# Kernel tuning notes

Measured on AMD Instinct MI355X. Metric: run time of the kernel, lower is better.

The kernel has to match this reference:

```python
import jax, jax.numpy as jnp
import numpy as np

NUM_EMBEDDINGS = 1024
EMBEDDING_DIM = 128
COMMITMENT_COST = 0.25


def setup_inputs() -> dict:
    key = jax.random.key(0)
    k_in, k_cb = jax.random.split(key)
    inputs = jax.random.normal(k_in, (65536, EMBEDDING_DIM), dtype=jnp.float32)
    # torch init: uniform(-1/K, 1/K)
    codebook = jax.random.uniform(
        k_cb, (NUM_EMBEDDINGS, EMBEDDING_DIM), dtype=jnp.float32,
        minval=-1.0 / NUM_EMBEDDINGS, maxval=1.0 / NUM_EMBEDDINGS)
    return {"inputs": inputs, "codebook": codebook}


def reference(inputs, codebook):
    # inputs: [N, D], codebook: [K, D]
    # squared euclidean distances [N, K]
    distances = (jnp.sum(inputs ** 2, axis=1, keepdims=True)
                 + jnp.sum(codebook ** 2, axis=1)
                 - 2.0 * jnp.matmul(inputs, codebook.T))
    encoding_indices = jnp.argmin(distances, axis=1)  # [N]
    encodings = jax.nn.one_hot(encoding_indices, NUM_EMBEDDINGS, dtype=jnp.float32)  # [N, K]
    # onehot @ codebook == gather
    quantized = jnp.take(codebook, encoding_indices, axis=0)  # [N, D]

    e_latent_loss = jnp.mean((jax.lax.stop_gradient(quantized) - inputs) ** 2)
    q_latent_loss = jnp.mean((quantized - jax.lax.stop_gradient(inputs)) ** 2)
    loss = q_latent_loss + COMMITMENT_COST * e_latent_loss

    # straight-through estimator
    quantized_st = inputs + jax.lax.stop_gradient(quantized - inputs)

    avg_probs = jnp.mean(encodings, axis=0)  # [K]
    perplexity = jnp.exp(-jnp.sum(avg_probs * jnp.log(avg_probs + 1e-10)))
    return (loss, quantized_st, perplexity, encodings)
```

## Files before the change

kernel.cpp:

```cpp
#include <hip/hip_runtime.h>

#define NROWS 65536
#define DIM   128
#define KC    1024
#define QST_OFF  1
#define PPL_OFF  8388609
#define ENC_OFF  8388610

typedef float f32x2 __attribute__((ext_vector_type(2)));
typedef float floatx4 __attribute__((ext_vector_type(4)));
typedef _Float16 half8_t __attribute__((ext_vector_type(8)));
typedef _Float16 half4_t __attribute__((ext_vector_type(4)));

#define BSTR 144
#define TILEH (64 * BSTR)
#define CHUNKH (2 * TILEH)

__device__ __forceinline__ float fadd_rn_(float a, float b) {
#pragma clang fp contract(off)
  return a + b;
}
__device__ __forceinline__ float fsub_rn_(float a, float b) {
#pragma clang fp contract(off)
  return a - b;
}
__device__ __forceinline__ float fmul_rn_(float a, float b) {
#pragma clang fp contract(off)
  return a * b;
}

__device__ __forceinline__ float rowsq128(const float4* src) {
  float r[8];
  {
    float4 v0 = src[0], v1 = src[1];
    r[0] = fmul_rn_(v0.x, v0.x); r[1] = fmul_rn_(v0.y, v0.y);
    r[2] = fmul_rn_(v0.z, v0.z); r[3] = fmul_rn_(v0.w, v0.w);
    r[4] = fmul_rn_(v1.x, v1.x); r[5] = fmul_rn_(v1.y, v1.y);
    r[6] = fmul_rn_(v1.z, v1.z); r[7] = fmul_rn_(v1.w, v1.w);
  }
  for (int i = 1; i < 16; ++i) {
    float4 v0 = src[2 * i], v1 = src[2 * i + 1];
    r[0] = fadd_rn_(r[0], fmul_rn_(v0.x, v0.x));
    r[1] = fadd_rn_(r[1], fmul_rn_(v0.y, v0.y));
    r[2] = fadd_rn_(r[2], fmul_rn_(v0.z, v0.z));
    r[3] = fadd_rn_(r[3], fmul_rn_(v0.w, v0.w));
    r[4] = fadd_rn_(r[4], fmul_rn_(v1.x, v1.x));
    r[5] = fadd_rn_(r[5], fmul_rn_(v1.y, v1.y));
    r[6] = fadd_rn_(r[6], fmul_rn_(v1.z, v1.z));
    r[7] = fadd_rn_(r[7], fmul_rn_(v1.w, v1.w));
  }
  return fadd_rn_(fadd_rn_(fadd_rn_(r[0], r[1]), fadd_rn_(r[2], r[3])),
                  fadd_rn_(fadd_rn_(r[4], r[5]), fadd_rn_(r[6], r[7])));
}

__global__ __launch_bounds__(256) void k_prep(const float* __restrict__ cb,
                                              float* __restrict__ cbT,
                                              float* __restrict__ cc,
                                              _Float16* __restrict__ Bp) {
  __shared__ float tile[64 * 129];
  int t = threadIdx.x;
  int c0 = blockIdx.x * 64;
#pragma unroll
  for (int it = 0; it < 32; ++it) {
    int f = it * 256 + t;
    int c = f >> 7, d = f & 127;
    tile[c * 129 + d] = cb[(size_t)(c0 + c) * DIM + d];
  }
  __syncthreads();
#pragma unroll
  for (int it = 0; it < 32; ++it) {
    int f = it * 256 + t;
    int d = f >> 6, c = f & 63;
    cbT[(size_t)d * KC + c0 + c] = tile[c * 129 + d];
  }
  if (t < 64) {
    const float* s = &tile[t * 129];
    float r[8];
#pragma unroll
    for (int j = 0; j < 8; ++j) r[j] = fmul_rn_(s[j], s[j]);
    for (int i = 1; i < 16; ++i) {
#pragma unroll
      for (int j = 0; j < 8; ++j)
        r[j] = fadd_rn_(r[j], fmul_rn_(s[i * 8 + j], s[i * 8 + j]));
    }
    cc[c0 + t] = fadd_rn_(fadd_rn_(fadd_rn_(r[0], r[1]), fadd_rn_(r[2], r[3])),
                          fadd_rn_(fadd_rn_(r[4], r[5]), fadd_rn_(r[6], r[7])));
  }
  size_t base = (size_t)blockIdx.x * CHUNKH;
#pragma unroll
  for (int it = 0; it < 32; ++it) {
    int f = it * 256 + t;
    int c = f >> 7, k = f & 127;
    float c5 = tile[c * 129 + k] * 512.0f;
    _Float16 h = (_Float16)c5;
    _Float16 l = (_Float16)(c5 - (float)h);
    Bp[base + c * BSTR + k] = h;
    Bp[base + TILEH + c * BSTR + k] = l;
  }
}

__global__ __launch_bounds__(256, 4) void k_main(const float* __restrict__ inp,
                                                 const float* __restrict__ cb,
                                                 const float* __restrict__ cbT,
                                                 const _Float16* __restrict__ Bp,
                                                 const float* __restrict__ cc,
                                                 float* __restrict__ out_qst,
                                                 float* __restrict__ out_enc,
                                                 int* __restrict__ cnt,
                                                 float* __restrict__ lsum) {
  __shared__ _Float16 SB[CHUNKH];
  __shared__ float xxs[64];
  __shared__ int bk[64];
  __shared__ int fl_rows[64];
  __shared__ int fl_cnt;
  __shared__ float xs[128];
  __shared__ float redd[4];
  __shared__ int redi[4];
  __shared__ float redf[4];

  int t = threadIdx.x;
  int lane = t & 63, w = t >> 6;
  int q = lane >> 4, col = lane & 15;
  int row0 = blockIdx.x * 64;
  if (t == 0) fl_cnt = 0;

  {
    int r = t & 63, seg = t >> 6;
    const float* src = inp + (size_t)(row0 + r) * DIM + seg * 32;
#pragma unroll
    for (int i = 0; i < 8; ++i) {
      float4 v = *(const float4*)(src + i * 4);
      _Float16 h0 = (_Float16)v.x, h1 = (_Float16)v.y, h2 = (_Float16)v.z, h3 = (_Float16)v.w;
      half4_t hv = {h0, h1, h2, h3};
      half4_t lv = {(_Float16)(v.x - (float)h0), (_Float16)(v.y - (float)h1),
                    (_Float16)(v.z - (float)h2), (_Float16)(v.w - (float)h3)};
      int k = seg * 32 + i * 4;
      *(half4_t*)&SB[r * BSTR + k] = hv;
      *(half4_t*)&SB[TILEH + r * BSTR + k] = lv;
    }
  }
  if (t < 64) xxs[t] = rowsq128((const float4*)(inp + (size_t)(row0 + t) * DIM));
  __syncthreads();

  int arow = w * 16 + col;
  half8_t ah[4], al[4];
#pragma unroll
  for (int ks = 0; ks < 4; ++ks) {
    ah[ks] = *(const half8_t*)&SB[arow * BSTR + ks * 32 + q * 8];
    al[ks] = *(const half8_t*)&SB[TILEH + arow * BSTR + ks * 32 + q * 8];
  }
  float xr[4];
#pragma unroll
  for (int r = 0; r < 4; ++r) xr[r] = xxs[w * 16 + q * 4 + r];

  float b1[4], b2[4];
  int i1[4];
#pragma unroll
  for (int r = 0; r < 4; ++r) { b1[r] = 3.4e38f; b2[r] = 3.4e38f; i1[r] = 0; }

  const float4* bp4 = (const float4*)Bp;

  for (int c = 0; c < 16; ++c) {
    __syncthreads();
    {
      float4 br[9];
#pragma unroll
      for (int r = 0; r < 9; ++r) br[r] = bp4[c * 2304 + r * 256 + t];
#pragma unroll
      for (int r = 0; r < 9; ++r) *(float4*)&SB[(size_t)(r * 256 + t) * 8] = br[r];
    }
    __syncthreads();

    float cck[4];
#pragma unroll
    for (int ct = 0; ct < 4; ++ct) cck[ct] = cc[c * 64 + ct * 16 + col];

    floatx4 acc[4];
#pragma unroll
    for (int ct = 0; ct < 4; ++ct) acc[ct] = (floatx4){0.f, 0.f, 0.f, 0.f};

#pragma unroll
    for (int ks = 0; ks < 4; ++ks) {
#pragma unroll
      for (int ct = 0; ct < 4; ++ct) {
        int brow = ct * 16 + col;
        half8_t bh = *(const half8_t*)&SB[brow * BSTR + ks * 32 + q * 8];
        half8_t bl = *(const half8_t*)&SB[TILEH + brow * BSTR + ks * 32 + q * 8];
        acc[ct] = __builtin_amdgcn_mfma_f32_16x16x32_f16(ah[ks], bh, acc[ct], 0, 0, 0);
        acc[ct] = __builtin_amdgcn_mfma_f32_16x16x32_f16(ah[ks], bl, acc[ct], 0, 0, 0);
        acc[ct] = __builtin_amdgcn_mfma_f32_16x16x32_f16(al[ks], bh, acc[ct], 0, 0, 0);
      }
    }

#pragma unroll
    for (int ct = 0; ct < 4; ++ct) {
#pragma unroll
      for (int r = 0; r < 4; ++r) {
        float m2 = fmul_rn_(acc[ct][r], 0.00390625f);
        float dist = fsub_rn_(fadd_rn_(xr[r], cck[ct]), m2);
        int kidx = c * 64 + ct * 16 + col;
        bool lt = dist < b1[r];
        b2[r] = lt ? b1[r] : fminf(b2[r], dist);
        i1[r] = lt ? kidx : i1[r];
        b1[r] = lt ? dist : b1[r];
      }
    }
  }

#pragma unroll
  for (int r = 0; r < 4; ++r) {
    float v1 = b1[r], v2 = b2[r];
    int ii = i1[r];
    for (int off = 1; off < 16; off <<= 1) {
      float ov1 = __shfl_xor(v1, off);
      float ov2 = __shfl_xor(v2, off);
      int oi = __shfl_xor(ii, off);
      float nb1 = fminf(v1, ov1);
      float nb2 = fminf(fmaxf(v1, ov1), fminf(v2, ov2));
      ii = (ov1 < v1) ? oi : ((ov1 > v1) ? ii : min(ii, oi));
      v1 = nb1; v2 = nb2;
    }
    b1[r] = v1; b2[r] = v2; i1[r] = ii;
  }

  if (col == 0) {
#pragma unroll
    for (int r = 0; r < 4; ++r) {
      int lrow = w * 16 + q * 4 + r;
      bk[lrow] = i1[r];
      float u = (b1[r] >= 256.f) ? 9.4e-5f : 4.7e-5f;
      if (b2[r] - b1[r] < u) {
        int p = atomicAdd(&fl_cnt, 1);
        fl_rows[p] = lrow;
      }
    }
  }
  __syncthreads();

  int nf = fl_cnt;
  for (int f = 0; f < nf; ++f) {
    int row = fl_rows[f];
    if (t < 128) xs[t] = inp[(size_t)(row0 + row) * DIM + t];
    __syncthreads();
    float xxr = xxs[row];
    int c0 = t * 4;
    float a0 = 0.f, a1 = 0.f, a2 = 0.f, a3 = 0.f;
    for (int d = 0; d < 128; ++d) {
      float xd = xs[d];
      float4 cv = *(const float4*)&cbT[(size_t)d * KC + c0];
      a0 = __builtin_fmaf(xd, cv.x, a0);
      a1 = __builtin_fmaf(xd, cv.y, a1);
      a2 = __builtin_fmaf(xd, cv.z, a2);
      a3 = __builtin_fmaf(xd, cv.w, a3);
    }
    float aa[4] = {a0, a1, a2, a3};
    float bb = 3.4e38f;
    int bi = 0;
#pragma unroll
    for (int j = 0; j < 4; ++j) {
      float dist = fsub_rn_(fadd_rn_(xxr, cc[c0 + j]), fmul_rn_(2.0f, aa[j]));
      if (dist < bb) { bb = dist; bi = c0 + j; }
    }
    for (int off = 1; off < 64; off <<= 1) {
      float ov = __shfl_xor(bb, off);
      int oi = __shfl_xor(bi, off);
      if (ov < bb || (ov == bb && oi < bi)) { bb = ov; bi = oi; }
    }
    if (lane == 0) { redd[w] = bb; redi[w] = bi; }
    __syncthreads();
    if (t == 0) {
      float vb = redd[0];
      int ib = redi[0];
#pragma unroll
      for (int ww = 1; ww < 4; ++ww) {
        if (redd[ww] < vb || (redd[ww] == vb && redi[ww] < ib)) { vb = redd[ww]; ib = redi[ww]; }
      }
      bk[row] = ib;
    }
    __syncthreads();
  }

  if (t < 64) atomicAdd(&cnt[bk[t]], 1);

  float ls = 0.f;
#pragma unroll 4
  for (int it = 0; it < 32; ++it) {
    int f = it * 256 + t;
    int row = f >> 7, d = f & 127;
    size_t gro = (size_t)(row0 + row) * DIM + d;
    float x = inp[gro];
    float qv = cb[(size_t)bk[row] * DIM + d];
    float qe = fsub_rn_(qv, x);
    out_qst[gro] = fadd_rn_(x, qe);
    ls = __builtin_fmaf(qe, qe, ls);
  }

  for (int it = 0; it < 128; ++it) {
    int f2 = it * 256 + t;
    int row = f2 >> 9, c2 = f2 & 511;
    int kk = bk[row];
    f32x2 v;
    v.x = (kk == 2 * c2) ? 1.0f : 0.0f;
    v.y = (kk == 2 * c2 + 1) ? 1.0f : 0.0f;
    *(f32x2*)&out_enc[(size_t)(row0 + row) * KC + 2 * c2] = v;
  }

  for (int off = 32; off; off >>= 1) ls += __shfl_down(ls, off);
  if (lane == 0) redf[w] = ls;
  __syncthreads();
  if (t == 0) atomicAdd(lsum, redf[0] + redf[1] + redf[2] + redf[3]);
}

__global__ __launch_bounds__(1024) void k_scalars(const int* __restrict__ cnt,
                                                  const float* __restrict__ lsum,
                                                  float* __restrict__ out) {
  int t = threadIdx.x;
  float p = (float)cnt[t] * (1.0f / 65536.0f);
  float term = fmul_rn_(p, logf(fadd_rn_(p, 1e-10f)));
  for (int off = 32; off; off >>= 1) term += __shfl_down(term, off);
  __shared__ float red[16];
  if ((t & 63) == 0) red[t >> 6] = term;
  __syncthreads();
  if (t == 0) {
    float s = 0.f;
#pragma unroll
    for (int w = 0; w < 16; ++w) s += red[w];
    out[PPL_OFF] = expf(-s);
    float e = *lsum * (1.0f / 8388608.0f);
    out[0] = fadd_rn_(e, fmul_rn_(0.25f, e));
  }
}

extern "C" void kernel_launch(void* const* d_in, const int* in_sizes, int n_in,
                              void* d_out, int out_size, void* d_ws, size_t ws_size,
                              hipStream_t stream) {
  const float* inp = (const float*)d_in[0];
  const float* cb = (const float*)d_in[1];
  float* out = (float*)d_out;

  _Float16* Bp = (_Float16*)d_ws;
  float* cbT = (float*)(Bp + 16 * CHUNKH);
  float* cc = cbT + DIM * KC;
  int* cnt = (int*)(cc + KC);
  float* lsum = (float*)(cnt + KC);

  (void)hipMemsetAsync(cnt, 0, (KC + 1) * sizeof(int), stream);
  k_prep<<<KC / 64, 256, 0, stream>>>(cb, cbT, cc, Bp);
  k_main<<<NROWS / 64, 256, 0, stream>>>(inp, cb, cbT, Bp, cc,
                                         out + QST_OFF, out + ENC_OFF, cnt, lsum);
  k_scalars<<<1, 1024, 0, stream>>>(cnt, lsum, out);
}
```

Baseline: 412.0 us.

## Double-buffer codebook chunks in LDS with register prefetch and smaller 32-code chunks

Restructures the main loop so codebook tiles are split into 32-row chunks stored in two LDS buffers. The next chunk is loaded from global memory into registers while the current chunk feeds the MFMAs, then written to the other buffer. This leaves one barrier per iteration instead of two. The goal is to hide global load latency behind compute, at the cost of twice as many loop iterations, fewer MFMAs per iteration and a changed workspace layout.

```diff
diff --git a/kernel.cpp b/kernel.cpp
--- a/kernel.cpp
+++ b/kernel.cpp
@@ -13,8 +13,10 @@
 typedef _Float16 half4_t __attribute__((ext_vector_type(4)));
 
 #define BSTR 144
-#define TILEH (64 * BSTR)
-#define CHUNKH (2 * TILEH)
+#define ALO  9216
+#define CH32 9216
+#define BLO  4608
+#define NCH  32
 
 __device__ __forceinline__ float fadd_rn_(float a, float b) {
 #pragma clang fp contract(off)
@@ -86,16 +88,18 @@
     cc[c0 + t] = fadd_rn_(fadd_rn_(fadd_rn_(r[0], r[1]), fadd_rn_(r[2], r[3])),
                           fadd_rn_(fadd_rn_(r[4], r[5]), fadd_rn_(r[6], r[7])));
   }
-  size_t base = (size_t)blockIdx.x * CHUNKH;
 #pragma unroll
   for (int it = 0; it < 32; ++it) {
     int f = it * 256 + t;
     int c = f >> 7, k = f & 127;
+    int gc = c0 + c;
+    int chunk = gc >> 5, cr = gc & 31;
     float c5 = tile[c * 129 + k] * 512.0f;
     _Float16 h = (_Float16)c5;
     _Float16 l = (_Float16)(c5 - (float)h);
-    Bp[base + c * BSTR + k] = h;
-    Bp[base + TILEH + c * BSTR + k] = l;
+    size_t base = (size_t)chunk * CH32;
+    Bp[base + cr * BSTR + k] = h;
+    Bp[base + BLO + cr * BSTR + k] = l;
   }
 }
 
@@ -108,7 +112,7 @@
                                                  float* __restrict__ out_enc,
                                                  int* __restrict__ cnt,
                                                  float* __restrict__ lsum) {
-  __shared__ _Float16 SB[CHUNKH];
+  __shared__ _Float16 SB[2 * CH32];
   __shared__ float xxs[64];
   __shared__ int bk[64];
   __shared__ int fl_rows[64];
@@ -136,7 +140,7 @@
                     (_Float16)(v.z - (float)h2), (_Float16)(v.w - (float)h3)};
       int k = seg * 32 + i * 4;
       *(half4_t*)&SB[r * BSTR + k] = hv;
-      *(half4_t*)&SB[TILEH + r * BSTR + k] = lv;
+      *(half4_t*)&SB[ALO + r * BSTR + k] = lv;
     }
   }
   if (t < 64) xxs[t] = rowsq128((const float4*)(inp + (size_t)(row0 + t) * DIM));
@@ -147,7 +151,7 @@
 #pragma unroll
   for (int ks = 0; ks < 4; ++ks) {
     ah[ks] = *(const half8_t*)&SB[arow * BSTR + ks * 32 + q * 8];
-    al[ks] = *(const half8_t*)&SB[TILEH + arow * BSTR + ks * 32 + q * 8];
+    al[ks] = *(const half8_t*)&SB[ALO + arow * BSTR + ks * 32 + q * 8];
   }
   float xr[4];
 #pragma unroll
@@ -159,33 +163,44 @@
   for (int r = 0; r < 4; ++r) { b1[r] = 3.4e38f; b2[r] = 3.4e38f; i1[r] = 0; }
 
   const float4* bp4 = (const float4*)Bp;
-
-  for (int c = 0; c < 16; ++c) {
-    __syncthreads();
-    {
-      float4 br[9];
-#pragma unroll
-      for (int r = 0; r < 9; ++r) br[r] = bp4[c * 2304 + r * 256 + t];
-#pragma unroll
-      for (int r = 0; r < 9; ++r) *(float4*)&SB[(size_t)(r * 256 + t) * 8] = br[r];
-    }
-    __syncthreads();
-
-    float cck[4];
-#pragma unroll
-    for (int ct = 0; ct < 4; ++ct) cck[ct] = cc[c * 64 + ct * 16 + col];
-
-    floatx4 acc[4];
-#pragma unroll
-    for (int ct = 0; ct < 4; ++ct) acc[ct] = (floatx4){0.f, 0.f, 0.f, 0.f};
+  float4* SBf4 = (float4*)SB;
+
+  float4 br[5];
+#pragma unroll
+  for (int r = 0; r < 4; ++r) br[r] = bp4[r * 256 + t];
+  if (t < 128) br[4] = bp4[1024 + t];
+
+  __syncthreads();
+
+#pragma unroll
+  for (int r = 0; r < 4; ++r) SBf4[r * 256 + t] = br[r];
+  if (t < 128) SBf4[1024 + t] = br[4];
+  __syncthreads();
+
+  for (int c = 0; c < NCH; ++c) {
+    const _Float16* cur = &SB[(c & 1) * CH32];
+
+    if (c < NCH - 1) {
+#pragma unroll
+      for (int r = 0; r < 4; ++r) br[r] = bp4[(c + 1) * 1152 + r * 256 + t];
+      if (t < 128) br[4] = bp4[(c + 1) * 1152 + 1024 + t];
+    }
+
+    float cck[2];
+#pragma unroll
+    for (int ct = 0; ct < 2; ++ct) cck[ct] = cc[c * 32 + ct * 16 + col];
+
+    floatx4 acc[2];
+#pragma unroll
+    for (int ct = 0; ct < 2; ++ct) acc[ct] = (floatx4){0.f, 0.f, 0.f, 0.f};
 
 #pragma unroll
     for (int ks = 0; ks < 4; ++ks) {
 #pragma unroll
-      for (int ct = 0; ct < 4; ++ct) {
+      for (int ct = 0; ct < 2; ++ct) {
         int brow = ct * 16 + col;
-        half8_t bh = *(const half8_t*)&SB[brow * BSTR + ks * 32 + q * 8];
-        half8_t bl = *(const half8_t*)&SB[TILEH + brow * BSTR + ks * 32 + q * 8];
+        half8_t bh = *(const half8_t*)&cur[brow * BSTR + ks * 32 + q * 8];
+        half8_t bl = *(const half8_t*)&cur[BLO + brow * BSTR + ks * 32 + q * 8];
         acc[ct] = __builtin_amdgcn_mfma_f32_16x16x32_f16(ah[ks], bh, acc[ct], 0, 0, 0);
         acc[ct] = __builtin_amdgcn_mfma_f32_16x16x32_f16(ah[ks], bl, acc[ct], 0, 0, 0);
         acc[ct] = __builtin_amdgcn_mfma_f32_16x16x32_f16(al[ks], bh, acc[ct], 0, 0, 0);
@@ -193,18 +208,26 @@
     }
 
 #pragma unroll
-    for (int ct = 0; ct < 4; ++ct) {
+    for (int ct = 0; ct < 2; ++ct) {
 #pragma unroll
       for (int r = 0; r < 4; ++r) {
         float m2 = fmul_rn_(acc[ct][r], 0.00390625f);
         float dist = fsub_rn_(fadd_rn_(xr[r], cck[ct]), m2);
-        int kidx = c * 64 + ct * 16 + col;
+        int kidx = c * 32 + ct * 16 + col;
         bool lt = dist < b1[r];
         b2[r] = lt ? b1[r] : fminf(b2[r], dist);
         i1[r] = lt ? kidx : i1[r];
         b1[r] = lt ? dist : b1[r];
       }
     }
+
+    if (c < NCH - 1) {
+      float4* dst = &SBf4[((c + 1) & 1) * 1152];
+#pragma unroll
+      for (int r = 0; r < 4; ++r) dst[r * 256 + t] = br[r];
+      if (t < 128) dst[1024 + t] = br[4];
+    }
+    __syncthreads();
   }
 
 #pragma unroll
@@ -339,7 +362,7 @@
   float* out = (float*)d_out;
 
   _Float16* Bp = (_Float16*)d_ws;
-  float* cbT = (float*)(Bp + 16 * CHUNKH);
+  float* cbT = (float*)(Bp + 32 * CH32);
   float* cc = cbT + DIM * KC;
   int* cnt = (int*)(cc + KC);
   float* lsum = (float*)(cnt + KC);
```

Measured after the change: 483.9 us. +17.4%, slower.
